# Kernel tuning notes

Hardware: AMD Instinct MI355X
Metric: run time of the kernel (lower is better)

The kernel has to match this reference:

```python
import jax, jax.numpy as jnp
import numpy as np

BIT_WIDTH = 8
QMAX = 2.0 ** (BIT_WIDTH - 1) - 1  # 127
QMIN = -(2.0 ** (BIT_WIDTH - 1))   # -128


def fake_quant(x, reduce_axes):
    """Symmetric int8 fake-quantization with per-channel abs-max scale.
    reduce_axes: axes reduced to compute the per-channel scale (channel dims kept).
    """
    scale = jnp.max(jnp.abs(x), axis=reduce_axes, keepdims=True) / QMAX
    scale = jnp.maximum(scale, 1e-8)
    q = jnp.clip(jnp.round(x / scale), QMIN, QMAX)
    return q * scale


def setup_inputs() -> dict:
    key = jax.random.key(0)
    ks = jax.random.split(key, 7)
    B, T, D = 4, 2048, 512
    return {
        "query": jax.random.normal(ks[0], (B, T, D), dtype=jnp.float32),
        "key": jax.random.normal(ks[1], (B, T, D), dtype=jnp.float32),
        "value": jax.random.normal(ks[2], (B, T, D), dtype=jnp.float32),
        "Wq": jax.random.normal(ks[3], (D, D), dtype=jnp.float32),
        "Wk": jax.random.normal(ks[4], (D, D), dtype=jnp.float32),
        "Wv": jax.random.normal(ks[5], (D, D), dtype=jnp.float32),
        "Wf": jax.random.normal(ks[6], (D, D), dtype=jnp.float32),
    }


def reference(query, key, value, Wq, Wk, Wv, Wf):
    H = 8
    B, T, D = query.shape
    dk = D // H

    # Activation fake-quant: per-token scale (stats over batch and feature dims)
    qx = fake_quant(query, (0, 2))
    kx = fake_quant(key, (0, 2))
    vx = fake_quant(value, (0, 2))
    # Weight fake-quant: per output column scale (stats over input rows)
    wq = fake_quant(Wq, (0,))
    wk = fake_quant(Wk, (0,))
    wv = fake_quant(Wv, (0,))

    def proj(x, w):  # [B,T,D] @ [D,D] -> [B,H,T,dk]
        return (x @ w).reshape(B, T, H, dk).transpose(0, 2, 1, 3)

    q = proj(qx, wq)
    k = proj(kx, wk)
    v = proj(vx, wv)

    scores = jnp.einsum("bhqd,bhkd->bhqk", q, k) / jnp.sqrt(jnp.float32(dk))
    p_attn = jax.nn.softmax(scores, axis=-1)  # dropout omitted (eval mode)
    x = jnp.einsum("bhqk,bhkd->bhqd", p_attn, v)
    x = x.transpose(0, 2, 1, 3).reshape(B, T, D)

    # Output activation quantized; weights_final is NOT quantized in the original forward
    out = fake_quant(x, (0, 2)) @ Wf
    return out
```

## Files before the change

kernel.cpp:

```cpp
#include <hip/hip_runtime.h>
#include <math.h>


typedef _Float16 f16x8 __attribute__((ext_vector_type(8)));
typedef _Float16 f16x2 __attribute__((ext_vector_type(2)));
typedef float f32x4 __attribute__((ext_vector_type(4)));
#define MFMA16(a, b, c) __builtin_amdgcn_mfma_f32_16x16x32_f16((a), (b), (c), 0, 0, 0)

__global__ __launch_bounds__(256) void token_scale(
    const float* __restrict__ x0, const float* __restrict__ x1,
    const float* __restrict__ x2, double* __restrict__ out)
{
    const int t = blockIdx.x;
    const int z = blockIdx.y;
    const float* __restrict__ x = (z == 0) ? x0 : ((z == 1) ? x1 : x2);
    const int tid = threadIdx.x;
    float m = 0.0f;
#pragma unroll
    for (int i = 0; i < 2; ++i) {
        int f = i * 256 + tid;
        int b = f >> 7, d4 = f & 127;
        float4 v = *(const float4*)(x + (long)(b * 2048 + t) * 512 + d4 * 4);
        m = fmaxf(m, fmaxf(fmaxf(fabsf(v.x), fabsf(v.y)), fmaxf(fabsf(v.z), fabsf(v.w))));
    }
#pragma unroll
    for (int off = 1; off < 64; off <<= 1) m = fmaxf(m, __shfl_xor(m, off));
    __shared__ float red[4];
    if ((tid & 63) == 0) red[tid >> 6] = m;
    __syncthreads();
    if (tid == 0) {
        m = fmaxf(fmaxf(red[0], red[1]), fmaxf(red[2], red[3]));
        out[z * 2048 + t] = fmax((double)m / 127.0, 1e-8);
    }
}

__global__ __launch_bounds__(256) void wquant(
    const float* __restrict__ Wq, const float* __restrict__ Wk,
    const float* __restrict__ Wv, double* __restrict__ sw,
    _Float16* __restrict__ qW)
{
    const int z = blockIdx.y;
    const float* __restrict__ W = (z == 0) ? Wq : (z == 1) ? Wk : Wv;
    const int col0 = blockIdx.x * 64;
    const int tid = threadIdx.x;
    const int c = tid & 63, kg = tid >> 6;

    __shared__ float redm[4][64];
    __shared__ double sS[64];
    __shared__ __align__(16) _Float16 qs[64][520];

    float m = 0.0f;
    for (int k = kg; k < 512; k += 4)
        m = fmaxf(m, fabsf(W[k * 512 + col0 + c]));
    redm[kg][c] = m;
    __syncthreads();
    if (tid < 64) {
        float mm = fmaxf(fmaxf(redm[0][tid], redm[1][tid]),
                         fmaxf(redm[2][tid], redm[3][tid]));
        double s = fmax((double)mm / 127.0, 1e-8);
        sw[z * 512 + col0 + tid] = s;
        sS[tid] = s;
    }
    __syncthreads();

    const double s = sS[c];
    for (int k = kg; k < 512; k += 4)
        qs[c][k] = (_Float16)fmin(fmax(rint((double)W[k * 512 + col0 + c] / s), -128.0), 127.0);
    __syncthreads();

    const int wc = tid >> 2, kc = (tid & 3) * 128;
    _Float16* q = qW + (long)z * 262144 + (long)(col0 + wc) * 512 + kc;
#pragma unroll
    for (int j = 0; j < 16; ++j)
        *(f16x8*)(q + j * 8) = *(const f16x8*)(&qs[wc][kc + j * 8]);
}

__global__ __launch_bounds__(256) void aquant(
    const float* __restrict__ x0, const float* __restrict__ x1,
    const float* __restrict__ x2, const double* __restrict__ sAll,
    _Float16* __restrict__ qA)
{
    const int z = blockIdx.y;
    const float* __restrict__ x = (z == 0) ? x0 : ((z == 1) ? x1 : x2);
    const double* __restrict__ s = sAll + z * 2048;
    const long PLANE = (long)4 * 2048 * 512;
    const long f = ((long)blockIdx.x * 256 + threadIdx.x) * 8;
    float4 v0 = *(const float4*)(x + f);
    float4 v1 = *(const float4*)(x + f + 4);
    const double sc = s[(f >> 9) & 2047];
    f16x8 q;
    q[0] = (_Float16)fmin(fmax(rint((double)v0.x / sc), -128.0), 127.0);
    q[1] = (_Float16)fmin(fmax(rint((double)v0.y / sc), -128.0), 127.0);
    q[2] = (_Float16)fmin(fmax(rint((double)v0.z / sc), -128.0), 127.0);
    q[3] = (_Float16)fmin(fmax(rint((double)v0.w / sc), -128.0), 127.0);
    q[4] = (_Float16)fmin(fmax(rint((double)v1.x / sc), -128.0), 127.0);
    q[5] = (_Float16)fmin(fmax(rint((double)v1.y / sc), -128.0), 127.0);
    q[6] = (_Float16)fmin(fmax(rint((double)v1.z / sc), -128.0), 127.0);
    q[7] = (_Float16)fmin(fmax(rint((double)v1.w / sc), -128.0), 127.0);
    *(f16x8*)(qA + (long)z * PLANE + f) = q;
}

__global__ __launch_bounds__(256) void wfsplit(
    const float* __restrict__ Wf, _Float16* __restrict__ WhT,
    _Float16* __restrict__ WlT)
{
    const int n0 = blockIdx.x * 64, k0 = blockIdx.y * 64;
    const int tid = threadIdx.x;
    __shared__ float T[64 * 68];
    {
        const int kr = tid >> 2, nc = (tid & 3) * 16;
#pragma unroll
        for (int j = 0; j < 4; ++j) {
            float4 v = *(const float4*)(Wf + (long)(k0 + kr) * 512 + n0 + nc + 4 * j);
            T[kr * 68 + nc + 4 * j + 0] = v.x;
            T[kr * 68 + nc + 4 * j + 1] = v.y;
            T[kr * 68 + nc + 4 * j + 2] = v.z;
            T[kr * 68 + nc + 4 * j + 3] = v.w;
        }
    }
    __syncthreads();
    const int nr = tid >> 2, kc = (tid & 3) * 16;
    f16x8 h[2], l[2];
#pragma unroll
    for (int j = 0; j < 16; ++j) {
        float wv = T[(kc + j) * 68 + nr];
        _Float16 hi = (_Float16)wv;
        h[j >> 3][j & 7] = hi;
        l[j >> 3][j & 7] = (_Float16)(wv - (float)hi);
    }
    *(f16x8*)(WhT + (long)(n0 + nr) * 512 + k0 + kc) = h[0];
    *(f16x8*)(WhT + (long)(n0 + nr) * 512 + k0 + kc + 8) = h[1];
    *(f16x8*)(WlT + (long)(n0 + nr) * 512 + k0 + kc) = l[0];
    *(f16x8*)(WlT + (long)(n0 + nr) * 512 + k0 + kc + 8) = l[1];
}

__global__ __launch_bounds__(256) void proj_mfma(
    const _Float16* __restrict__ qA, const _Float16* __restrict__ qW,
    const double* __restrict__ saAll, const double* __restrict__ swAll,
    _Float16* __restrict__ Qh, _Float16* __restrict__ Ql,
    _Float16* __restrict__ Kh, _Float16* __restrict__ Kl,
    _Float16* __restrict__ Vh, _Float16* __restrict__ Vl,
    int b)
{
    const int z = blockIdx.z;
    const _Float16* __restrict__ A = qA + ((long)z * 4 + b) * (2048l * 512);
    const _Float16* __restrict__ Bq = qW + (long)z * 262144;
    const double* __restrict__ sa = saAll + z * 2048;
    const double* __restrict__ swz = swAll + z * 512;

    const int m0 = blockIdx.x * 64, n0 = blockIdx.y * 64;
    const int tid = threadIdx.x;
    const int w = tid >> 6, lane = tid & 63;
    const int ln = lane & 15, quad = lane >> 4;

    __shared__ __align__(16) _Float16 As[64 * 72];
    __shared__ __align__(16) _Float16 Bs[64 * 72];
    const int srow = tid >> 3, scs = (tid & 7) * 8;

    f32x4 c[4];
#pragma unroll
    for (int nt = 0; nt < 4; ++nt) { c[nt][0] = 0; c[nt][1] = 0; c[nt][2] = 0; c[nt][3] = 0; }

    f16x8 a0, a1, b0, b1;
    a0 = *(const f16x8*)(A + (long)(m0 + srow) * 512 + scs);
    a1 = *(const f16x8*)(A + (long)(m0 + 32 + srow) * 512 + scs);
    b0 = *(const f16x8*)(Bq + (long)(n0 + srow) * 512 + scs);
    b1 = *(const f16x8*)(Bq + (long)(n0 + 32 + srow) * 512 + scs);

    for (int k0 = 0; k0 < 512; k0 += 64) {
        __syncthreads();
        *(f16x8*)(As + srow * 72 + scs) = a0;
        *(f16x8*)(As + (32 + srow) * 72 + scs) = a1;
        *(f16x8*)(Bs + srow * 72 + scs) = b0;
        *(f16x8*)(Bs + (32 + srow) * 72 + scs) = b1;
        __syncthreads();
        if (k0 + 64 < 512) {
            a0 = *(const f16x8*)(A + (long)(m0 + srow) * 512 + k0 + 64 + scs);
            a1 = *(const f16x8*)(A + (long)(m0 + 32 + srow) * 512 + k0 + 64 + scs);
            b0 = *(const f16x8*)(Bq + (long)(n0 + srow) * 512 + k0 + 64 + scs);
            b1 = *(const f16x8*)(Bq + (long)(n0 + 32 + srow) * 512 + k0 + 64 + scs);
        }
#pragma unroll
        for (int ks = 0; ks < 2; ++ks) {
            f16x8 aF = *(const f16x8*)(As + (w * 16 + ln) * 72 + ks * 32 + quad * 8);
#pragma unroll
            for (int nt = 0; nt < 4; ++nt) {
                f16x8 bF = *(const f16x8*)(Bs + (nt * 16 + ln) * 72 + ks * 32 + quad * 8);
                c[nt] = MFMA16(aF, bF, c[nt]);
            }
        }
    }

#pragma unroll
    for (int nt = 0; nt < 4; ++nt)
#pragma unroll
        for (int r = 0; r < 4; ++r) {
            int t = m0 + w * 16 + quad * 4 + r;
            int n = n0 + nt * 16 + ln;
            float val = (float)((double)c[nt][r] * sa[t] * swz[n]);
            _Float16 hi = (_Float16)val;
            _Float16 lo = (_Float16)(val - (float)hi);
            int hh = n >> 6, d = n & 63;
            if (z == 2) {
                long idx = ((long)hh * 64 + d) * 2048 + t;
                Vh[idx] = hi; Vl[idx] = lo;
            } else if (z == 1) {
                long idx = ((long)hh * 2048 + t) * 64 + d;
                Kh[idx] = hi; Kl[idx] = lo;
            } else {
                long idx = ((long)hh * 2048 + t) * 64 + d;
                Qh[idx] = hi; Ql[idx] = lo;
            }
        }
}

__global__ __launch_bounds__(256) void attn_mfma(
    const _Float16* __restrict__ Qh0, const _Float16* __restrict__ Ql0,
    const _Float16* __restrict__ Kh0, const _Float16* __restrict__ Kl0,
    const _Float16* __restrict__ Vh0, const _Float16* __restrict__ Vl0,
    float* __restrict__ xbuf, int bbase)
{
    const int wg = blockIdx.x + (blockIdx.y << 5) + (blockIdx.z << 8);
    const int xcd = wg & 7, j = wg >> 3;
    const int pair = (xcd << 1) + (j >> 5);
    const int q0 = (j & 31) * 64;
    const int h = pair >> 1;
    const int slot = pair & 1;
    const int b = bbase + slot;

    const long PE = (long)8 * 2048 * 64;
    const _Float16* __restrict__ Qh = Qh0 + (long)slot * PE;
    const _Float16* __restrict__ Ql = Ql0 + (long)slot * PE;
    const _Float16* __restrict__ Kh = Kh0 + (long)slot * PE;
    const _Float16* __restrict__ Kl = Kl0 + (long)slot * PE;
    const _Float16* __restrict__ Vh = Vh0 + (long)slot * PE;
    const _Float16* __restrict__ Vl = Vl0 + (long)slot * PE;

    const int tid = threadIdx.x;
    const int w = tid >> 6, lane = tid & 63;
    const int ln = lane & 15, quad = lane >> 4;

    __shared__ __align__(16) _Float16 KsH[64 * 72];
    __shared__ __align__(16) _Float16 KsL[64 * 72];
    __shared__ __align__(16) _Float16 VsH[64 * 72];
    __shared__ __align__(16) _Float16 VsL[64 * 72];
    __shared__ __align__(16) _Float16 PTh[4][16 * 72];
    __shared__ __align__(16) _Float16 PTl[4][16 * 72];

    f16x8 qh[2], ql[2];
    {
        const long r = ((long)h * 2048 + q0 + w * 16 + ln) * 64 + quad * 8;
        qh[0] = *(const f16x8*)(Qh + r);
        qh[1] = *(const f16x8*)(Qh + r + 32);
        ql[0] = *(const f16x8*)(Ql + r);
        ql[1] = *(const f16x8*)(Ql + r + 32);
    }

    float m_run = -INFINITY, l_run = 0.0f;

    f32x4 O[4];
#pragma unroll
    for (int dt = 0; dt < 4; ++dt) { O[dt][0] = 0; O[dt][1] = 0; O[dt][2] = 0; O[dt][3] = 0; }

    const int srow = tid >> 3, scs = (tid & 7) * 8;
    const long kBase = (long)h * 2048;
    const long vBase = (long)h * 64;
    f16x8 sg0, sg1, sg2, sg3, sg4, sg5, sg6, sg7;
    sg0 = *(const f16x8*)(Kh + (kBase + 0 + srow) * 64 + scs);
    sg1 = *(const f16x8*)(Kh + (kBase + 0 + 32 + srow) * 64 + scs);
    sg2 = *(const f16x8*)(Kl + (kBase + 0 + srow) * 64 + scs);
    sg3 = *(const f16x8*)(Kl + (kBase + 0 + 32 + srow) * 64 + scs);
    sg4 = *(const f16x8*)(Vh + (vBase + srow) * 2048 + 0 + scs);
    sg5 = *(const f16x8*)(Vh + (vBase + 32 + srow) * 2048 + 0 + scs);
    sg6 = *(const f16x8*)(Vl + (vBase + srow) * 2048 + 0 + scs);
    sg7 = *(const f16x8*)(Vl + (vBase + 32 + srow) * 2048 + 0 + scs);

    for (int k0 = 0; k0 < 2048; k0 += 64) {
        __syncthreads();
        *(f16x8*)(KsH + srow * 72 + scs)        = sg0;
        *(f16x8*)(KsH + (32 + srow) * 72 + scs) = sg1;
        *(f16x8*)(KsL + srow * 72 + scs)        = sg2;
        *(f16x8*)(KsL + (32 + srow) * 72 + scs) = sg3;
        *(f16x8*)(VsH + srow * 72 + scs)        = sg4;
        *(f16x8*)(VsH + (32 + srow) * 72 + scs) = sg5;
        *(f16x8*)(VsL + srow * 72 + scs)        = sg6;
        *(f16x8*)(VsL + (32 + srow) * 72 + scs) = sg7;
        __syncthreads();
        if (k0 + 64 < 2048) {
            const int kn = k0 + 64;
            sg0 = *(const f16x8*)(Kh + (kBase + kn + srow) * 64 + scs);
            sg1 = *(const f16x8*)(Kh + (kBase + kn + 32 + srow) * 64 + scs);
            sg2 = *(const f16x8*)(Kl + (kBase + kn + srow) * 64 + scs);
            sg3 = *(const f16x8*)(Kl + (kBase + kn + 32 + srow) * 64 + scs);
            sg4 = *(const f16x8*)(Vh + (vBase + srow) * 2048 + kn + scs);
            sg5 = *(const f16x8*)(Vh + (vBase + 32 + srow) * 2048 + kn + scs);
            sg6 = *(const f16x8*)(Vl + (vBase + srow) * 2048 + kn + scs);
            sg7 = *(const f16x8*)(Vl + (vBase + 32 + srow) * 2048 + kn + scs);
        }

        f32x4 sT[4];
        __builtin_amdgcn_s_setprio(1);
#pragma unroll
        for (int kt = 0; kt < 4; ++kt) {
            f32x4 s; s[0] = 0; s[1] = 0; s[2] = 0; s[3] = 0;
#pragma unroll
            for (int ks = 0; ks < 2; ++ks) {
                const int off = (kt * 16 + ln) * 72 + ks * 32 + quad * 8;
                f16x8 kh = *(const f16x8*)(KsH + off);
                f16x8 kl = *(const f16x8*)(KsL + off);
                s = MFMA16(kl, qh[ks], s);
                s = MFMA16(kh, ql[ks], s);
                s = MFMA16(kh, qh[ks], s);
            }
            sT[kt] = s;
        }
        __builtin_amdgcn_s_setprio(0);

        float rm = -INFINITY;
#pragma unroll
        for (int kt = 0; kt < 4; ++kt)
#pragma unroll
            for (int r = 0; r < 4; ++r) rm = fmaxf(rm, sT[kt][r]);
        rm = fmaxf(rm, __shfl_xor(rm, 16));
        rm = fmaxf(rm, __shfl_xor(rm, 32));
        const float mn = fmaxf(m_run, rm);
        const float a = __expf((m_run - mn) * 0.125f);
        m_run = mn;

        float sum = 0.0f;
#pragma unroll
        for (int kt = 0; kt < 4; ++kt) {
#pragma unroll
            for (int r = 0; r < 4; r += 2) {
                float p0 = __expf((sT[kt][r]     - mn) * 0.125f);
                float p1 = __expf((sT[kt][r + 1] - mn) * 0.125f);
                sum += p0 + p1;
                float s0 = p0 * 512.0f, s1 = p1 * 512.0f;
                _Float16 h0 = (_Float16)s0, h1 = (_Float16)s1;
                f16x2 hp = {h0, h1};
                f16x2 lp = {(_Float16)(s0 - (float)h0), (_Float16)(s1 - (float)h1)};
                const int poff = ln * 72 + kt * 16 + quad * 4 + r;
                *(f16x2*)(&PTh[w][poff]) = hp;
                *(f16x2*)(&PTl[w][poff]) = lp;
            }
        }
        sum += __shfl_xor(sum, 16);
        sum += __shfl_xor(sum, 32);
        l_run = l_run * a + sum;

#pragma unroll
        for (int dt = 0; dt < 4; ++dt) {
            O[dt][0] *= a; O[dt][1] *= a; O[dt][2] *= a; O[dt][3] *= a;
        }

        __builtin_amdgcn_s_setprio(1);
#pragma unroll
        for (int ks2 = 0; ks2 < 2; ++ks2) {
            f16x8 ph = *(const f16x8*)(&PTh[w][ln * 72 + ks2 * 32 + quad * 8]);
            f16x8 pl = *(const f16x8*)(&PTl[w][ln * 72 + ks2 * 32 + quad * 8]);
#pragma unroll
            for (int dt = 0; dt < 4; ++dt) {
                const int off = (dt * 16 + ln) * 72 + ks2 * 32 + quad * 8;
                f16x8 vh = *(const f16x8*)(VsH + off);
                f16x8 vl = *(const f16x8*)(VsL + off);
                O[dt] = MFMA16(vh, pl, O[dt]);
                O[dt] = MFMA16(vl, ph, O[dt]);
                O[dt] = MFMA16(vh, ph, O[dt]);
            }
        }
        __builtin_amdgcn_s_setprio(0);
    }

    const float inv = 1.0f / (512.0f * l_run);
    const long base = ((long)(b * 2048 + q0 + w * 16 + ln)) * 512 + h * 64 + quad * 4;
#pragma unroll
    for (int dt = 0; dt < 4; ++dt) {
        float4 o;
        o.x = O[dt][0] * inv; o.y = O[dt][1] * inv;
        o.z = O[dt][2] * inv; o.w = O[dt][3] * inv;
        *(float4*)(xbuf + base + dt * 16) = o;
    }
}

__global__ __launch_bounds__(256) void final_mfma(
    const _Float16* __restrict__ qX, const _Float16* __restrict__ WhT,
    const _Float16* __restrict__ WlT, const double* __restrict__ sx,
    float* __restrict__ out)
{
    const int m0 = blockIdx.x * 64, n0 = blockIdx.y * 64;
    const int tid = threadIdx.x;
    const int w = tid >> 6, lane = tid & 63;
    const int ln = lane & 15, quad = lane >> 4;

    __shared__ __align__(16) _Float16 As[64 * 72];
    __shared__ __align__(16) _Float16 BhS[64 * 72];
    __shared__ __align__(16) _Float16 BlS[64 * 72];
    const int srow = tid >> 3, scs = (tid & 7) * 8;

    f32x4 c[4];
#pragma unroll
    for (int nt = 0; nt < 4; ++nt) { c[nt][0] = 0; c[nt][1] = 0; c[nt][2] = 0; c[nt][3] = 0; }

    f16x8 a0, a1, h0, h1, l0, l1;
    a0 = *(const f16x8*)(qX + (long)(m0 + srow) * 512 + scs);
    a1 = *(const f16x8*)(qX + (long)(m0 + 32 + srow) * 512 + scs);
    h0 = *(const f16x8*)(WhT + (long)(n0 + srow) * 512 + scs);
    h1 = *(const f16x8*)(WhT + (long)(n0 + 32 + srow) * 512 + scs);
    l0 = *(const f16x8*)(WlT + (long)(n0 + srow) * 512 + scs);
    l1 = *(const f16x8*)(WlT + (long)(n0 + 32 + srow) * 512 + scs);

    for (int k0 = 0; k0 < 512; k0 += 64) {
        __syncthreads();
        *(f16x8*)(As + srow * 72 + scs) = a0;
        *(f16x8*)(As + (32 + srow) * 72 + scs) = a1;
        *(f16x8*)(BhS + srow * 72 + scs) = h0;
        *(f16x8*)(BhS + (32 + srow) * 72 + scs) = h1;
        *(f16x8*)(BlS + srow * 72 + scs) = l0;
        *(f16x8*)(BlS + (32 + srow) * 72 + scs) = l1;
        __syncthreads();
        if (k0 + 64 < 512) {
            a0 = *(const f16x8*)(qX + (long)(m0 + srow) * 512 + k0 + 64 + scs);
            a1 = *(const f16x8*)(qX + (long)(m0 + 32 + srow) * 512 + k0 + 64 + scs);
            h0 = *(const f16x8*)(WhT + (long)(n0 + srow) * 512 + k0 + 64 + scs);
            h1 = *(const f16x8*)(WhT + (long)(n0 + 32 + srow) * 512 + k0 + 64 + scs);
            l0 = *(const f16x8*)(WlT + (long)(n0 + srow) * 512 + k0 + 64 + scs);
            l1 = *(const f16x8*)(WlT + (long)(n0 + 32 + srow) * 512 + k0 + 64 + scs);
        }
#pragma unroll
        for (int ks = 0; ks < 2; ++ks) {
            f16x8 aF = *(const f16x8*)(As + (w * 16 + ln) * 72 + ks * 32 + quad * 8);
#pragma unroll
            for (int nt = 0; nt < 4; ++nt) {
                const int off = (nt * 16 + ln) * 72 + ks * 32 + quad * 8;
                f16x8 bh = *(const f16x8*)(BhS + off);
                f16x8 bl = *(const f16x8*)(BlS + off);
                c[nt] = MFMA16(aF, bl, c[nt]);
                c[nt] = MFMA16(aF, bh, c[nt]);
            }
        }
    }

#pragma unroll
    for (int nt = 0; nt < 4; ++nt)
#pragma unroll
        for (int r = 0; r < 4; ++r) {
            int m = m0 + w * 16 + quad * 4 + r;
            int n = n0 + nt * 16 + ln;
            out[(long)m * 512 + n] = (float)((double)c[nt][r] * sx[m & 2047]);
        }
}

extern "C" void kernel_launch(void* const* d_in, const int* in_sizes, int n_in,
                              void* d_out, int out_size, void* d_ws, size_t ws_size,
                              hipStream_t stream)
{
    const float* query = (const float*)d_in[0];
    const float* key_  = (const float*)d_in[1];
    const float* value = (const float*)d_in[2];
    const float* Wq = (const float*)d_in[3];
    const float* Wk = (const float*)d_in[4];
    const float* Wv = (const float*)d_in[5];
    const float* Wf = (const float*)d_in[6];
    float* out = (float*)d_out;

    char* p = (char*)d_ws;
    auto alloc = [&](size_t bytes) -> char* {
        char* r = p;
        p += (bytes + 255) & ~(size_t)255;
        return r;
    };
    double*   sA   = (double*)alloc(3 * 2048 * 8);
    double*   sx   = (double*)alloc(2048 * 8);
    double*   sw   = (double*)alloc(3 * 512 * 8);
    _Float16* qW   = (_Float16*)alloc((size_t)3 * 512 * 512 * 2);
    const long PE  = (long)8 * 2048 * 64;
    _Float16* Qh   = (_Float16*)alloc((size_t)2 * PE * 2);
    _Float16* Ql   = (_Float16*)alloc((size_t)2 * PE * 2);
    _Float16* Kh   = (_Float16*)alloc((size_t)2 * PE * 2);
    _Float16* Kl   = (_Float16*)alloc((size_t)2 * PE * 2);
    _Float16* Vh   = (_Float16*)alloc((size_t)2 * PE * 2);
    _Float16* Vl   = (_Float16*)alloc((size_t)2 * PE * 2);
    float*    xbuf = (float*)alloc((size_t)8192 * 512 * 4);
    _Float16* qA   = (_Float16*)alloc((size_t)3 * 4 * 2048 * 512 * 2);
    _Float16* WhT  = (_Float16*)alloc((size_t)512 * 512 * 2);
    _Float16* WlT  = (_Float16*)alloc((size_t)512 * 512 * 2);

    token_scale<<<dim3(2048, 3), 256, 0, stream>>>(query, key_, value, sA);
    wquant<<<dim3(8, 3), 256, 0, stream>>>(Wq, Wk, Wv, sw, qW);
    aquant<<<dim3(2048, 3), 256, 0, stream>>>(query, key_, value, sA, qA);
    wfsplit<<<dim3(8, 8), 256, 0, stream>>>(Wf, WhT, WlT);
    for (int pair = 0; pair < 2; ++pair) {
        proj_mfma<<<dim3(32, 8, 3), 256, 0, stream>>>(qA, qW, sA, sw,
            Qh, Ql, Kh, Kl, Vh, Vl, pair * 2);
        proj_mfma<<<dim3(32, 8, 3), 256, 0, stream>>>(qA, qW, sA, sw,
            Qh + PE, Ql + PE, Kh + PE, Kl + PE, Vh + PE, Vl + PE, pair * 2 + 1);
        attn_mfma<<<dim3(32, 8, 2), 256, 0, stream>>>(Qh, Ql, Kh, Kl, Vh, Vl, xbuf, pair * 2);
    }
    token_scale<<<dim3(2048, 1), 256, 0, stream>>>(xbuf, xbuf, xbuf, sx);
    aquant<<<dim3(2048, 1), 256, 0, stream>>>(xbuf, xbuf, xbuf, sx, qA);
    final_mfma<<<dim3(128, 8), 256, 0, stream>>>(qA, WhT, WlT, sx, out);
}
```

Before: 416.7 us.

## Shrink attention blocks to two waves, XOR-swizzle LDS tiles, remap head scheduling

```diff
diff --git a/kernel.cpp b/kernel.cpp
--- a/kernel.cpp
+++ b/kernel.cpp
@@ -214,18 +214,17 @@
         }
 }
 
-__global__ __launch_bounds__(256) void attn_mfma(
+__global__ __launch_bounds__(128, 2) void attn_mfma(
     const _Float16* __restrict__ Qh0, const _Float16* __restrict__ Ql0,
     const _Float16* __restrict__ Kh0, const _Float16* __restrict__ Kl0,
     const _Float16* __restrict__ Vh0, const _Float16* __restrict__ Vl0,
     float* __restrict__ xbuf, int bbase)
 {
-    const int wg = blockIdx.x + (blockIdx.y << 5) + (blockIdx.z << 8);
-    const int xcd = wg & 7, j = wg >> 3;
-    const int pair = (xcd << 1) + (j >> 5);
-    const int q0 = (j & 31) * 64;
-    const int h = pair >> 1;
-    const int slot = pair & 1;
+    const int wg = blockIdx.x + (blockIdx.y << 6) + (blockIdx.z << 9);
+    const int h = wg & 7;
+    const int j = wg >> 3;
+    const int slot = j >> 6;
+    const int q0 = (j & 63) * 32;
     const int b = bbase + slot;
 
     const long PE = (long)8 * 2048 * 64;
@@ -239,13 +238,14 @@
     const int tid = threadIdx.x;
     const int w = tid >> 6, lane = tid & 63;
     const int ln = lane & 15, quad = lane >> 4;
-
-    __shared__ __align__(16) _Float16 KsH[64 * 72];
-    __shared__ __align__(16) _Float16 KsL[64 * 72];
-    __shared__ __align__(16) _Float16 VsH[64 * 72];
-    __shared__ __align__(16) _Float16 VsL[64 * 72];
-    __shared__ __align__(16) _Float16 PTh[4][16 * 72];
-    __shared__ __align__(16) _Float16 PTl[4][16 * 72];
+    const int swz = ln & 7;
+
+    __shared__ __align__(16) _Float16 KsH[64 * 64];
+    __shared__ __align__(16) _Float16 KsL[64 * 64];
+    __shared__ __align__(16) _Float16 VsH[64 * 64];
+    __shared__ __align__(16) _Float16 VsL[64 * 64];
+    __shared__ __align__(16) _Float16 PTh[2][16 * 64];
+    __shared__ __align__(16) _Float16 PTl[2][16 * 64];
 
     f16x8 qh[2], ql[2];
     {
@@ -262,40 +262,39 @@
 #pragma unroll
     for (int dt = 0; dt < 4; ++dt) { O[dt][0] = 0; O[dt][1] = 0; O[dt][2] = 0; O[dt][3] = 0; }
 
-    const int srow = tid >> 3, scs = (tid & 7) * 8;
+    const int trow = tid >> 3, tcs = tid & 7;
+    const int tsl = ((tcs ^ (trow & 7)) << 3);
     const long kBase = (long)h * 2048;
     const long vBase = (long)h * 64;
-    f16x8 sg0, sg1, sg2, sg3, sg4, sg5, sg6, sg7;
-    sg0 = *(const f16x8*)(Kh + (kBase + 0 + srow) * 64 + scs);
-    sg1 = *(const f16x8*)(Kh + (kBase + 0 + 32 + srow) * 64 + scs);
-    sg2 = *(const f16x8*)(Kl + (kBase + 0 + srow) * 64 + scs);
-    sg3 = *(const f16x8*)(Kl + (kBase + 0 + 32 + srow) * 64 + scs);
-    sg4 = *(const f16x8*)(Vh + (vBase + srow) * 2048 + 0 + scs);
-    sg5 = *(const f16x8*)(Vh + (vBase + 32 + srow) * 2048 + 0 + scs);
-    sg6 = *(const f16x8*)(Vl + (vBase + srow) * 2048 + 0 + scs);
-    sg7 = *(const f16x8*)(Vl + (vBase + 32 + srow) * 2048 + 0 + scs);
+    f16x8 sg[16];
+#pragma unroll
+    for (int pp = 0; pp < 4; ++pp) {
+        sg[pp * 4 + 0] = *(const f16x8*)(Kh + (kBase + trow + 16 * pp) * 64 + tcs * 8);
+        sg[pp * 4 + 1] = *(const f16x8*)(Kl + (kBase + trow + 16 * pp) * 64 + tcs * 8);
+        sg[pp * 4 + 2] = *(const f16x8*)(Vh + (vBase + trow + 16 * pp) * 2048 + tcs * 8);
+        sg[pp * 4 + 3] = *(const f16x8*)(Vl + (vBase + trow + 16 * pp) * 2048 + tcs * 8);
+    }
 
     for (int k0 = 0; k0 < 2048; k0 += 64) {
         __syncthreads();
-        *(f16x8*)(KsH + srow * 72 + scs)        = sg0;
-        *(f16x8*)(KsH + (32 + srow) * 72 + scs) = sg1;
-        *(f16x8*)(KsL + srow * 72 + scs)        = sg2;
-        *(f16x8*)(KsL + (32 + srow) * 72 + scs) = sg3;
-        *(f16x8*)(VsH + srow * 72 + scs)        = sg4;
-        *(f16x8*)(VsH + (32 + srow) * 72 + scs) = sg5;
-        *(f16x8*)(VsL + srow * 72 + scs)        = sg6;
-        *(f16x8*)(VsL + (32 + srow) * 72 + scs) = sg7;
+#pragma unroll
+        for (int pp = 0; pp < 4; ++pp) {
+            const int li = (trow + 16 * pp) * 64 + tsl;
+            *(f16x8*)(KsH + li) = sg[pp * 4 + 0];
+            *(f16x8*)(KsL + li) = sg[pp * 4 + 1];
+            *(f16x8*)(VsH + li) = sg[pp * 4 + 2];
+            *(f16x8*)(VsL + li) = sg[pp * 4 + 3];
+        }
         __syncthreads();
         if (k0 + 64 < 2048) {
             const int kn = k0 + 64;
-            sg0 = *(const f16x8*)(Kh + (kBase + kn + srow) * 64 + scs);
-            sg1 = *(const f16x8*)(Kh + (kBase + kn + 32 + srow) * 64 + scs);
-            sg2 = *(const f16x8*)(Kl + (kBase + kn + srow) * 64 + scs);
-            sg3 = *(const f16x8*)(Kl + (kBase + kn + 32 + srow) * 64 + scs);
-            sg4 = *(const f16x8*)(Vh + (vBase + srow) * 2048 + kn + scs);
-            sg5 = *(const f16x8*)(Vh + (vBase + 32 + srow) * 2048 + kn + scs);
-            sg6 = *(const f16x8*)(Vl + (vBase + srow) * 2048 + kn + scs);
-            sg7 = *(const f16x8*)(Vl + (vBase + 32 + srow) * 2048 + kn + scs);
+#pragma unroll
+            for (int pp = 0; pp < 4; ++pp) {
+                sg[pp * 4 + 0] = *(const f16x8*)(Kh + (kBase + kn + trow + 16 * pp) * 64 + tcs * 8);
+                sg[pp * 4 + 1] = *(const f16x8*)(Kl + (kBase + kn + trow + 16 * pp) * 64 + tcs * 8);
+                sg[pp * 4 + 2] = *(const f16x8*)(Vh + (vBase + trow + 16 * pp) * 2048 + kn + tcs * 8);
+                sg[pp * 4 + 3] = *(const f16x8*)(Vl + (vBase + trow + 16 * pp) * 2048 + kn + tcs * 8);
+            }
         }
 
         f32x4 sT[4];
@@ -305,7 +304,7 @@
             f32x4 s; s[0] = 0; s[1] = 0; s[2] = 0; s[3] = 0;
 #pragma unroll
             for (int ks = 0; ks < 2; ++ks) {
-                const int off = (kt * 16 + ln) * 72 + ks * 32 + quad * 8;
+                const int off = (kt * 16 + ln) * 64 + (((ks * 4 + quad) ^ swz) << 3);
                 f16x8 kh = *(const f16x8*)(KsH + off);
                 f16x8 kl = *(const f16x8*)(KsL + off);
                 s = MFMA16(kl, qh[ks], s);
@@ -339,7 +338,8 @@
                 _Float16 h0 = (_Float16)s0, h1 = (_Float16)s1;
                 f16x2 hp = {h0, h1};
                 f16x2 lp = {(_Float16)(s0 - (float)h0), (_Float16)(s1 - (float)h1)};
-                const int poff = ln * 72 + kt * 16 + quad * 4 + r;
+                const int cb = (kt * 32 + quad * 8 + 2 * r) ^ (swz << 4);
+                const int poff = ln * 64 + (cb >> 1);
                 *(f16x2*)(&PTh[w][poff]) = hp;
                 *(f16x2*)(&PTl[w][poff]) = lp;
             }
@@ -356,11 +356,12 @@
         __builtin_amdgcn_s_setprio(1);
 #pragma unroll
         for (int ks2 = 0; ks2 < 2; ++ks2) {
-            f16x8 ph = *(const f16x8*)(&PTh[w][ln * 72 + ks2 * 32 + quad * 8]);
-            f16x8 pl = *(const f16x8*)(&PTl[w][ln * 72 + ks2 * 32 + quad * 8]);
+            const int psl = (((ks2 * 4 + quad) ^ swz) << 3);
+            f16x8 ph = *(const f16x8*)(&PTh[w][ln * 64 + psl]);
+            f16x8 pl = *(const f16x8*)(&PTl[w][ln * 64 + psl]);
 #pragma unroll
             for (int dt = 0; dt < 4; ++dt) {
-                const int off = (dt * 16 + ln) * 72 + ks2 * 32 + quad * 8;
+                const int off = (dt * 16 + ln) * 64 + psl;
                 f16x8 vh = *(const f16x8*)(VsH + off);
                 f16x8 vl = *(const f16x8*)(VsL + off);
                 O[dt] = MFMA16(vh, pl, O[dt]);
@@ -494,7 +495,7 @@
             Qh, Ql, Kh, Kl, Vh, Vl, pair * 2);
         proj_mfma<<<dim3(32, 8, 3), 256, 0, stream>>>(qA, qW, sA, sw,
             Qh + PE, Ql + PE, Kh + PE, Kl + PE, Vh + PE, Vl + PE, pair * 2 + 1);
-        attn_mfma<<<dim3(32, 8, 2), 256, 0, stream>>>(Qh, Ql, Kh, Kl, Vh, Vl, xbuf, pair * 2);
+        attn_mfma<<<dim3(64, 8, 2), 128, 0, stream>>>(Qh, Ql, Kh, Kl, Vh, Vl, xbuf, pair * 2);
     }
     token_scale<<<dim3(2048, 1), 256, 0, stream>>>(xbuf, xbuf, xbuf, sx);
     aquant<<<dim3(2048, 1), 256, 0, stream>>>(xbuf, xbuf, xbuf, sx, qA);
```

Result: slower. 428.9 us (+2.9%).

## Software-pipeline attention loop with double-buffered swizzled K/V shared tiles

Applied to the files above, without the earlier changes.

```diff
diff --git a/kernel.cpp b/kernel.cpp
--- a/kernel.cpp
+++ b/kernel.cpp
@@ -239,13 +239,14 @@
     const int tid = threadIdx.x;
     const int w = tid >> 6, lane = tid & 63;
     const int ln = lane & 15, quad = lane >> 4;
-
-    __shared__ __align__(16) _Float16 KsH[64 * 72];
-    __shared__ __align__(16) _Float16 KsL[64 * 72];
-    __shared__ __align__(16) _Float16 VsH[64 * 72];
-    __shared__ __align__(16) _Float16 VsL[64 * 72];
-    __shared__ __align__(16) _Float16 PTh[4][16 * 72];
-    __shared__ __align__(16) _Float16 PTl[4][16 * 72];
+    const int swz = ln & 7;
+
+    __shared__ __align__(16) _Float16 KsH[2][4096];
+    __shared__ __align__(16) _Float16 KsL[2][4096];
+    __shared__ __align__(16) _Float16 VsH[2][4096];
+    __shared__ __align__(16) _Float16 VsL[2][4096];
+    __shared__ __align__(16) _Float16 PTh[4][1024];
+    __shared__ __align__(16) _Float16 PTl[4][1024];
 
     f16x8 qh[2], ql[2];
     {
@@ -257,57 +258,44 @@
     }
 
     float m_run = -INFINITY, l_run = 0.0f;
-
     f32x4 O[4];
 #pragma unroll
     for (int dt = 0; dt < 4; ++dt) { O[dt][0] = 0; O[dt][1] = 0; O[dt][2] = 0; O[dt][3] = 0; }
 
     const int srow = tid >> 3, scs = (tid & 7) * 8;
+    const int tsl = (((tid & 7) ^ (srow & 7)) << 3);
     const long kBase = (long)h * 2048;
     const long vBase = (long)h * 64;
     f16x8 sg0, sg1, sg2, sg3, sg4, sg5, sg6, sg7;
-    sg0 = *(const f16x8*)(Kh + (kBase + 0 + srow) * 64 + scs);
-    sg1 = *(const f16x8*)(Kh + (kBase + 0 + 32 + srow) * 64 + scs);
-    sg2 = *(const f16x8*)(Kl + (kBase + 0 + srow) * 64 + scs);
-    sg3 = *(const f16x8*)(Kl + (kBase + 0 + 32 + srow) * 64 + scs);
-    sg4 = *(const f16x8*)(Vh + (vBase + srow) * 2048 + 0 + scs);
-    sg5 = *(const f16x8*)(Vh + (vBase + 32 + srow) * 2048 + 0 + scs);
-    sg6 = *(const f16x8*)(Vl + (vBase + srow) * 2048 + 0 + scs);
-    sg7 = *(const f16x8*)(Vl + (vBase + 32 + srow) * 2048 + 0 + scs);
-
-    for (int k0 = 0; k0 < 2048; k0 += 64) {
-        __syncthreads();
-        *(f16x8*)(KsH + srow * 72 + scs)        = sg0;
-        *(f16x8*)(KsH + (32 + srow) * 72 + scs) = sg1;
-        *(f16x8*)(KsL + srow * 72 + scs)        = sg2;
-        *(f16x8*)(KsL + (32 + srow) * 72 + scs) = sg3;
-        *(f16x8*)(VsH + srow * 72 + scs)        = sg4;
-        *(f16x8*)(VsH + (32 + srow) * 72 + scs) = sg5;
-        *(f16x8*)(VsL + srow * 72 + scs)        = sg6;
-        *(f16x8*)(VsL + (32 + srow) * 72 + scs) = sg7;
-        __syncthreads();
-        if (k0 + 64 < 2048) {
-            const int kn = k0 + 64;
-            sg0 = *(const f16x8*)(Kh + (kBase + kn + srow) * 64 + scs);
-            sg1 = *(const f16x8*)(Kh + (kBase + kn + 32 + srow) * 64 + scs);
-            sg2 = *(const f16x8*)(Kl + (kBase + kn + srow) * 64 + scs);
-            sg3 = *(const f16x8*)(Kl + (kBase + kn + 32 + srow) * 64 + scs);
-            sg4 = *(const f16x8*)(Vh + (vBase + srow) * 2048 + kn + scs);
-            sg5 = *(const f16x8*)(Vh + (vBase + 32 + srow) * 2048 + kn + scs);
-            sg6 = *(const f16x8*)(Vl + (vBase + srow) * 2048 + kn + scs);
-            sg7 = *(const f16x8*)(Vl + (vBase + 32 + srow) * 2048 + kn + scs);
-        }
-
-        f32x4 sT[4];
+
+    auto LOADT = [&](int kt) {
+        sg0 = *(const f16x8*)(Kh + (kBase + kt + srow) * 64 + scs);
+        sg1 = *(const f16x8*)(Kh + (kBase + kt + 32 + srow) * 64 + scs);
+        sg2 = *(const f16x8*)(Kl + (kBase + kt + srow) * 64 + scs);
+        sg3 = *(const f16x8*)(Kl + (kBase + kt + 32 + srow) * 64 + scs);
+        sg4 = *(const f16x8*)(Vh + (vBase + srow) * 2048 + kt + scs);
+        sg5 = *(const f16x8*)(Vh + (vBase + 32 + srow) * 2048 + kt + scs);
+        sg6 = *(const f16x8*)(Vl + (vBase + srow) * 2048 + kt + scs);
+        sg7 = *(const f16x8*)(Vl + (vBase + 32 + srow) * 2048 + kt + scs);
+    };
+    auto STORET = [&](int bs) {
+        const int li  = srow * 64 + tsl;
+        const int li2 = (32 + srow) * 64 + tsl;
+        *(f16x8*)(&KsH[bs][li])  = sg0;  *(f16x8*)(&KsH[bs][li2]) = sg1;
+        *(f16x8*)(&KsL[bs][li])  = sg2;  *(f16x8*)(&KsL[bs][li2]) = sg3;
+        *(f16x8*)(&VsH[bs][li])  = sg4;  *(f16x8*)(&VsH[bs][li2]) = sg5;
+        *(f16x8*)(&VsL[bs][li])  = sg6;  *(f16x8*)(&VsL[bs][li2]) = sg7;
+    };
+    auto STEP_S = [&](int bs, f32x4* sT) {
         __builtin_amdgcn_s_setprio(1);
 #pragma unroll
         for (int kt = 0; kt < 4; ++kt) {
             f32x4 s; s[0] = 0; s[1] = 0; s[2] = 0; s[3] = 0;
 #pragma unroll
             for (int ks = 0; ks < 2; ++ks) {
-                const int off = (kt * 16 + ln) * 72 + ks * 32 + quad * 8;
-                f16x8 kh = *(const f16x8*)(KsH + off);
-                f16x8 kl = *(const f16x8*)(KsL + off);
+                const int off = (kt * 16 + ln) * 64 + (((ks * 4 + quad) ^ swz) << 3);
+                f16x8 kh = *(const f16x8*)(&KsH[bs][off]);
+                f16x8 kl = *(const f16x8*)(&KsL[bs][off]);
                 s = MFMA16(kl, qh[ks], s);
                 s = MFMA16(kh, ql[ks], s);
                 s = MFMA16(kh, qh[ks], s);
@@ -315,7 +303,27 @@
             sT[kt] = s;
         }
         __builtin_amdgcn_s_setprio(0);
-
+    };
+    auto STEP_PV = [&](int bs) {
+        __builtin_amdgcn_s_setprio(1);
+#pragma unroll
+        for (int ks2 = 0; ks2 < 2; ++ks2) {
+            const int psl = (((ks2 * 4 + quad) ^ swz) << 3);
+            f16x8 ph = *(const f16x8*)(&PTh[w][ln * 64 + psl]);
+            f16x8 pl = *(const f16x8*)(&PTl[w][ln * 64 + psl]);
+#pragma unroll
+            for (int dt = 0; dt < 4; ++dt) {
+                const int off = (dt * 16 + ln) * 64 + psl;
+                f16x8 vh = *(const f16x8*)(&VsH[bs][off]);
+                f16x8 vl = *(const f16x8*)(&VsL[bs][off]);
+                O[dt] = MFMA16(vh, pl, O[dt]);
+                O[dt] = MFMA16(vl, ph, O[dt]);
+                O[dt] = MFMA16(vh, ph, O[dt]);
+            }
+        }
+        __builtin_amdgcn_s_setprio(0);
+    };
+    auto STEP_SM = [&](f32x4* sT) {
         float rm = -INFINITY;
 #pragma unroll
         for (int kt = 0; kt < 4; ++kt)
@@ -326,7 +334,6 @@
         const float mn = fmaxf(m_run, rm);
         const float a = __expf((m_run - mn) * 0.125f);
         m_run = mn;
-
         float sum = 0.0f;
 #pragma unroll
         for (int kt = 0; kt < 4; ++kt) {
@@ -339,7 +346,8 @@
                 _Float16 h0 = (_Float16)s0, h1 = (_Float16)s1;
                 f16x2 hp = {h0, h1};
                 f16x2 lp = {(_Float16)(s0 - (float)h0), (_Float16)(s1 - (float)h1)};
-                const int poff = ln * 72 + kt * 16 + quad * 4 + r;
+                const int cb = (kt * 32 + quad * 8 + 2 * r) ^ (swz << 4);
+                const int poff = ln * 64 + (cb >> 1);
                 *(f16x2*)(&PTh[w][poff]) = hp;
                 *(f16x2*)(&PTl[w][poff]) = lp;
             }
@@ -347,29 +355,38 @@
         sum += __shfl_xor(sum, 16);
         sum += __shfl_xor(sum, 32);
         l_run = l_run * a + sum;
-
 #pragma unroll
         for (int dt = 0; dt < 4; ++dt) {
             O[dt][0] *= a; O[dt][1] *= a; O[dt][2] *= a; O[dt][3] *= a;
         }
-
-        __builtin_amdgcn_s_setprio(1);
-#pragma unroll
-        for (int ks2 = 0; ks2 < 2; ++ks2) {
-            f16x8 ph = *(const f16x8*)(&PTh[w][ln * 72 + ks2 * 32 + quad * 8]);
-            f16x8 pl = *(const f16x8*)(&PTl[w][ln * 72 + ks2 * 32 + quad * 8]);
-#pragma unroll
-            for (int dt = 0; dt < 4; ++dt) {
-                const int off = (dt * 16 + ln) * 72 + ks2 * 32 + quad * 8;
-                f16x8 vh = *(const f16x8*)(VsH + off);
-                f16x8 vl = *(const f16x8*)(VsL + off);
-                O[dt] = MFMA16(vh, pl, O[dt]);
-                O[dt] = MFMA16(vl, ph, O[dt]);
-                O[dt] = MFMA16(vh, ph, O[dt]);
-            }
-        }
-        __builtin_amdgcn_s_setprio(0);
-    }
+    };
+
+    LOADT(0);
+    STORET(0);
+    __syncthreads();
+    LOADT(64);
+    {
+        f32x4 sT[4];
+        STEP_S(0, sT);
+        STEP_SM(sT);
+    }
+    STORET(1);
+    __syncthreads();
+    LOADT(128);
+    int cur = 1;
+
+    for (int k0 = 64; k0 < 2048; k0 += 64) {
+        f32x4 sT[4];
+        STEP_S(cur, sT);
+        STEP_PV(cur ^ 1);
+        STEP_SM(sT);
+        __syncthreads();
+        if (k0 + 64 < 2048) STORET(cur ^ 1);
+        __syncthreads();
+        if (k0 + 128 < 2048) LOADT(k0 + 128);
+        cur ^= 1;
+    }
+    STEP_PV(cur ^ 1);
 
     const float inv = 1.0f / (512.0f * l_run);
     const long base = ((long)(b * 2048 + q0 + w * 16 + ln)) * 512 + h * 64 + quad * 4;
```

Measured after the change: 404.7 us. -2.9%, faster.
